# Kernel optimization log

Hardware: AMD Instinct MI355X
Metric: run time of the kernel (lower is better)

The kernel has to match this reference:

```python
import jax, jax.numpy as jnp
import numpy as np

N_NODES = 100000


def _spmm(edge_src, edge_dst, edge_vals, support):
    # out[i] = sum_{e: dst(e)=i} w_e * support[src(e)]  (sparse adj @ support)
    msgs = support[edge_src] * edge_vals[:, None]  # [E, F]
    return jax.ops.segment_sum(msgs, edge_dst, num_segments=N_NODES)


def setup_inputs() -> dict:
    key = jax.random.key(0)
    ks = jax.random.split(key, 8)
    E = 1600000
    feat_dim, nhid, num_class = 256, 64, 16
    x = jax.random.normal(ks[0], (N_NODES, feat_dim), dtype=jnp.float32)
    edge_src = jax.random.randint(ks[1], (E,), 0, N_NODES, dtype=jnp.int32)
    edge_dst = jax.random.randint(ks[2], (E,), 0, N_NODES, dtype=jnp.int32)
    edge_vals = jax.random.uniform(ks[3], (E,), dtype=jnp.float32)
    # Glorot-style init as in the original GraphConvolution.reset_parameters
    W1 = jax.random.normal(ks[4], (feat_dim, nhid), dtype=jnp.float32) / np.sqrt(feat_dim)
    b1 = jnp.zeros((nhid,), dtype=jnp.float32)
    W2 = jax.random.normal(ks[5], (nhid, num_class), dtype=jnp.float32) / np.sqrt(nhid)
    b2 = jnp.zeros((num_class,), dtype=jnp.float32)
    return {"x": x, "edge_src": edge_src, "edge_dst": edge_dst,
            "edge_vals": edge_vals, "W1": W1, "b1": b1, "W2": W2, "b2": b2}


def reference(x, edge_src, edge_dst, edge_vals, W1, b1, W2, b2):
    # gc1: support = x @ W1 ; out = adj @ support + b1 ; relu
    h = jax.nn.relu(_spmm(edge_src, edge_dst, edge_vals, x @ W1) + b1)
    # dropout is identity in eval mode (training=False)
    # gc2
    logits = _spmm(edge_src, edge_dst, edge_vals, h @ W2) + b2
    return jax.nn.log_softmax(logits, axis=1)
```

## Files before the change

kernel.cpp:

```cpp
#include <hip/hip_runtime.h>
#include <hip/hip_fp16.h>

#define N_NODES 100000
#define E_EDGES 1600000
#define F_IN    256
#define F_HID   64
#define F_OUT   16
#define NBKT    391
#define CAP     4608
#define GEMM1_BLOCKS 782
#define PA_BLOCKS    782

typedef _Float16 half8   __attribute__((ext_vector_type(8)));
typedef _Float16 half2v  __attribute__((ext_vector_type(2)));
typedef float    floatx4 __attribute__((ext_vector_type(4)));

__global__ __launch_bounds__(256) void prep_kernel(const float* __restrict__ W1,
                                                   _Float16* __restrict__ W1h,
                                                   int* __restrict__ bucketCursor) {
    const int i = blockIdx.x * 256 + threadIdx.x;
    if (i < NBKT) bucketCursor[i] = 0;
    const int k = i >> 6, n = i & 63;
    const int kb = k >> 5, quad = (k >> 3) & 3, j = k & 7;
    const int nt = n >> 4, ln = n & 15;
    W1h[((kb * 4 + nt) * 64 + quad * 16 + ln) * 8 + j] = (_Float16)W1[i];
}

__global__ __launch_bounds__(256) void gemm1_passA_kernel(const float* __restrict__ x,
                                                          const _Float16* __restrict__ W1h,
                                                          _Float16* __restrict__ support1,
                                                          const int* __restrict__ esrc,
                                                          const int* __restrict__ edst,
                                                          const float* __restrict__ evals,
                                                          int* __restrict__ bucketCursor,
                                                          int2* __restrict__ tmp) {
    __shared__ int hist[NBKT];
    __shared__ int base[NBKT];
    const int t = threadIdx.x;

    if (blockIdx.x >= GEMM1_BLOCKS) {
        const int blk = blockIdx.x - GEMM1_BLOCKS;
        for (int i = t; i < NBKT; i += 256) hist[i] = 0;
        __syncthreads();
        const int base_e = blk * 2048;
        int rks[2][4];
#pragma unroll
        for (int ch = 0; ch < 2; ++ch) {
            const int e0 = base_e + ch * 1024 + t * 4;
            if (e0 < E_EDGES) {
                int4 d4 = *(const int4*)&edst[e0];
                rks[ch][0] = atomicAdd(&hist[d4.x >> 8], 1);
                rks[ch][1] = atomicAdd(&hist[d4.y >> 8], 1);
                rks[ch][2] = atomicAdd(&hist[d4.z >> 8], 1);
                rks[ch][3] = atomicAdd(&hist[d4.w >> 8], 1);
            }
        }
        __syncthreads();
        for (int i = t; i < NBKT; i += 256) {
            const int h = hist[i];
            if (h) base[i] = atomicAdd(&bucketCursor[i], h);
        }
        __syncthreads();
#pragma unroll
        for (int ch = 0; ch < 2; ++ch) {
            const int e0 = base_e + ch * 1024 + t * 4;
            if (e0 < E_EDGES) {
                int4 d4 = *(const int4*)&edst[e0];
                int4 s4 = *(const int4*)&esrc[e0];
                float4 v4 = *(const float4*)&evals[e0];
                const int dd[4] = {d4.x, d4.y, d4.z, d4.w};
                const int ss[4] = {s4.x, s4.y, s4.z, s4.w};
                const float vv[4] = {v4.x, v4.y, v4.z, v4.w};
#pragma unroll
                for (int u = 0; u < 4; ++u) {
                    const int bu = dd[u] >> 8;
                    const int bpos = base[bu] + rks[ch][u];
                    if (bpos < CAP)
                        tmp[(size_t)bu * CAP + bpos] =
                            make_int2(((dd[u] & 255) << 17) | ss[u],
                                      __float_as_int(vv[u]));
                }
            }
        }
        return;
    }

    const int wave = t >> 6;
    const int lane = t & 63;
    const int ln   = lane & 15;
    const int quad = lane >> 4;
    const int row0 = blockIdx.x * 128 + wave * 32;

    const float* xp[2];
#pragma unroll
    for (int mt = 0; mt < 2; ++mt) {
        int r = row0 + mt * 16 + ln;
        if (r > N_NODES - 1) r = N_NODES - 1;
        xp[mt] = x + (size_t)r * F_IN + quad * 8;
    }

    floatx4 acc[2][4] = {};

#pragma unroll 4
    for (int kb = 0; kb < 8; ++kb) {
        half8 a[2];
#pragma unroll
        for (int mt = 0; mt < 2; ++mt) {
            float4 v0 = *(const float4*)(xp[mt] + kb * 32);
            float4 v1 = *(const float4*)(xp[mt] + kb * 32 + 4);
            half8 h;
            h[0] = (_Float16)v0.x; h[1] = (_Float16)v0.y;
            h[2] = (_Float16)v0.z; h[3] = (_Float16)v0.w;
            h[4] = (_Float16)v1.x; h[5] = (_Float16)v1.y;
            h[6] = (_Float16)v1.z; h[7] = (_Float16)v1.w;
            a[mt] = h;
        }
#pragma unroll
        for (int nt = 0; nt < 4; ++nt) {
            half8 b = *(const half8*)&W1h[((size_t)((kb * 4 + nt) * 64 + lane)) * 8];
            acc[0][nt] = __builtin_amdgcn_mfma_f32_16x16x32_f16(a[0], b, acc[0][nt], 0, 0, 0);
            acc[1][nt] = __builtin_amdgcn_mfma_f32_16x16x32_f16(a[1], b, acc[1][nt], 0, 0, 0);
        }
    }

#pragma unroll
    for (int mt = 0; mt < 2; ++mt) {
        const int rbase = row0 + mt * 16 + quad * 4;
#pragma unroll
        for (int r = 0; r < 4; ++r) {
            const int row = rbase + r;
            if (row < N_NODES) {
#pragma unroll
                for (int nt = 0; nt < 4; ++nt)
                    support1[(size_t)row * F_HID + nt * 16 + ln] = (_Float16)acc[mt][nt][r];
            }
        }
    }
}

__global__ __launch_bounds__(256) void passB_kernel(const int2* __restrict__ tmp,
                                                    const int* __restrict__ bucketCursor,
                                                    int2* __restrict__ sorted_edges,
                                                    int* __restrict__ rowstart,
                                                    int* __restrict__ deg) {
    __shared__ int ldeg[256];
    __shared__ int lcur[256];
    __shared__ int s[256];
    const int t = threadIdx.x;
    const int b = blockIdx.x;
    const int beg = b * CAP;
    int cnt = bucketCursor[b];
    if (cnt > CAP) cnt = CAP;

    ldeg[t] = 0;
    __syncthreads();

    for (int p = t; p < cnt; p += 256) {
        int2 r = tmp[beg + p];
        atomicAdd(&ldeg[r.x >> 17], 1);
    }
    __syncthreads();

    const int v = ldeg[t];
    s[t] = v;
    __syncthreads();
#pragma unroll
    for (int off = 1; off < 256; off <<= 1) {
        const int y = (t >= off) ? s[t - off] : 0;
        __syncthreads();
        s[t] += y;
        __syncthreads();
    }
    const int run = s[t] - v;
    lcur[t] = run;
    const int node = b * 256 + t;
    if (node < N_NODES) { rowstart[node] = beg + run; deg[node] = v; }
    __syncthreads();

    for (int p = t; p < cnt; p += 256) {
        int2 r = tmp[beg + p];
        const int pos = beg + atomicAdd(&lcur[r.x >> 17], 1);
        sorted_edges[pos] = make_int2(r.x & 0x1FFFF, r.y);
    }
}

__global__ __launch_bounds__(256) void spmm1_fused_kernel(const int* __restrict__ rowstart,
                                                          const int* __restrict__ deg,
                                                          const int2* __restrict__ sorted_edges,
                                                          const _Float16* __restrict__ support1,
                                                          const float* __restrict__ b1,
                                                          const float* __restrict__ W2,
                                                          _Float16* __restrict__ support2) {
    __shared__ float W2s[64 * 17];
    __shared__ float b1s[64];
    __shared__ __align__(16) float hs[4][64];
    const int t = threadIdx.x;
    for (int i = t; i < 1024; i += 256)
        W2s[(i >> 4) * 17 + (i & 15)] = W2[i];
    if (t < 64) b1s[t] = b1[t];
    __syncthreads();

    const int wave = t >> 6;
    const int lane = t & 63;
    const int node = blockIdx.x * 4 + wave;
    const int c4 = lane & 15;
    const int q  = lane >> 4;

    const int beg = rowstart[node];
    const int cnt = deg[node];

    int   src_l = 0;
    float val_l = 0.f;
    if (lane < cnt) {
        int2 ev = sorted_edges[beg + lane];
        src_l = ev.x;
        val_l = __int_as_float(ev.y);
    }

    half2v a01 = {(_Float16)0, (_Float16)0};
    half2v a23 = {(_Float16)0, (_Float16)0};
    const int kmax  = cnt < 64 ? cnt : 64;
    const int quads = (kmax + 3) >> 2;
    const int qp    = (quads + 3) & ~3;
    for (int k = 0; k < qp; k += 4) {
        float w[4]; uint2 d[4];
#pragma unroll
        for (int u = 0; u < 4; ++u) {
            const int idx = 4 * (k + u) + q;
            const int s2  = __shfl(src_l, idx);
            w[u] = __shfl(val_l, idx);
            d[u] = *(const uint2*)&support1[(s2 << 6) + 4 * c4];
        }
#pragma unroll
        for (int u = 0; u < 4; ++u) {
            const half2v* hp = (const half2v*)&d[u];
            const _Float16 wh = (_Float16)w[u];
            const half2v w2 = {wh, wh};
            a01 += w2 * hp[0];
            a23 += w2 * hp[1];
        }
    }
    for (int k = 64 + q; k < cnt; k += 4) {
        int2 ev = sorted_edges[beg + k];
        const uint2 d = *(const uint2*)&support1[(ev.x << 6) + 4 * c4];
        const half2v* hp = (const half2v*)&d;
        const _Float16 wh = (_Float16)__int_as_float(ev.y);
        const half2v w2 = {wh, wh};
        a01 += w2 * hp[0];
        a23 += w2 * hp[1];
    }

    float acc0 = (float)a01[0], acc1 = (float)a01[1];
    float acc2 = (float)a23[0], acc3 = (float)a23[1];
    acc0 += __shfl_xor(acc0, 16); acc0 += __shfl_xor(acc0, 32);
    acc1 += __shfl_xor(acc1, 16); acc1 += __shfl_xor(acc1, 32);
    acc2 += __shfl_xor(acc2, 16); acc2 += __shfl_xor(acc2, 32);
    acc3 += __shfl_xor(acc3, 16); acc3 += __shfl_xor(acc3, 32);
    if (q == 0) {
        float4 hv;
        hv.x = fmaxf(acc0 + b1s[4 * c4],     0.f);
        hv.y = fmaxf(acc1 + b1s[4 * c4 + 1], 0.f);
        hv.z = fmaxf(acc2 + b1s[4 * c4 + 2], 0.f);
        hv.w = fmaxf(acc3 + b1s[4 * c4 + 3], 0.f);
        *(float4*)&hs[wave][4 * c4] = hv;
    }
    __syncthreads();

    const int ln   = lane & 15;
    const int quad = lane >> 4;
    float o = 0.f;
#pragma unroll
    for (int kk = 0; kk < 16; ++kk) {
        const int k2 = quad * 16 + kk;
        o = fmaf(hs[wave][k2], W2s[k2 * 17 + ln], o);
    }
    o += __shfl_xor(o, 16);
    o += __shfl_xor(o, 32);
    if (quad == 0)
        support2[(size_t)node * F_OUT + ln] = (_Float16)o;
}

__global__ __launch_bounds__(256) void spmm2_fused_kernel(const int* __restrict__ rowstart,
                                                          const int* __restrict__ deg,
                                                          const int2* __restrict__ sorted_edges,
                                                          const _Float16* __restrict__ support2,
                                                          const float* __restrict__ b2,
                                                          float* __restrict__ out) {
    __shared__ float b2s[16];
    const int t = threadIdx.x;
    if (t < 16) b2s[t] = b2[t];
    __syncthreads();

    const int j    = t & 15;
    const int node = blockIdx.x * 16 + (t >> 4);
    const int c = j & 3;
    const int p = j >> 2;

    const int beg = rowstart[node];
    const int cnt = deg[node];

    int   src_a = 0, src_b = 0;
    float val_a = 0.f, val_b = 0.f;
    if (j < cnt)      { int2 ev = sorted_edges[beg + j];      src_a = ev.x; val_a = __int_as_float(ev.y); }
    if (j + 16 < cnt) { int2 ev = sorted_edges[beg + 16 + j]; src_b = ev.x; val_b = __int_as_float(ev.y); }

    half2v a01 = {(_Float16)0, (_Float16)0};
    half2v a23 = {(_Float16)0, (_Float16)0};
    {
        float w[4]; uint2 d[4];
#pragma unroll
        for (int u = 0; u < 4; ++u) {
            const int idx = 4 * u + p;
            const int s2  = __shfl(src_a, idx, 16);
            w[u] = __shfl(val_a, idx, 16);
            d[u] = *(const uint2*)&support2[(s2 << 4) + 4 * c];
        }
#pragma unroll
        for (int u = 0; u < 4; ++u) {
            const half2v* hp = (const half2v*)&d[u];
            const _Float16 wh = (_Float16)w[u];
            const half2v w2 = {wh, wh};
            a01 += w2 * hp[0];
            a23 += w2 * hp[1];
        }
    }
    if (cnt > 16) {
        float w[4]; uint2 d[4];
#pragma unroll
        for (int u = 0; u < 4; ++u) {
            const int idx = 4 * u + p;
            const int s2  = __shfl(src_b, idx, 16);
            w[u] = __shfl(val_b, idx, 16);
            d[u] = *(const uint2*)&support2[(s2 << 4) + 4 * c];
        }
#pragma unroll
        for (int u = 0; u < 4; ++u) {
            const half2v* hp = (const half2v*)&d[u];
            const _Float16 wh = (_Float16)w[u];
            const half2v w2 = {wh, wh};
            a01 += w2 * hp[0];
            a23 += w2 * hp[1];
        }
    }
    for (int k = 32 + p; k < cnt; k += 4) {
        int2 ev = sorted_edges[beg + k];
        const uint2 d = *(const uint2*)&support2[(ev.x << 4) + 4 * c];
        const half2v* hp = (const half2v*)&d;
        const _Float16 wh = (_Float16)__int_as_float(ev.y);
        const half2v w2 = {wh, wh};
        a01 += w2 * hp[0];
        a23 += w2 * hp[1];
    }

    float acc0 = (float)a01[0], acc1 = (float)a01[1];
    float acc2 = (float)a23[0], acc3 = (float)a23[1];
    acc0 += __shfl_xor(acc0, 4, 16); acc0 += __shfl_xor(acc0, 8, 16);
    acc1 += __shfl_xor(acc1, 4, 16); acc1 += __shfl_xor(acc1, 8, 16);
    acc2 += __shfl_xor(acc2, 4, 16); acc2 += __shfl_xor(acc2, 8, 16);
    acc3 += __shfl_xor(acc3, 4, 16); acc3 += __shfl_xor(acc3, 8, 16);

    const float v0 = acc0 + b2s[4 * c];
    const float v1 = acc1 + b2s[4 * c + 1];
    const float v2 = acc2 + b2s[4 * c + 2];
    const float v3 = acc3 + b2s[4 * c + 3];
    float m = fmaxf(fmaxf(v0, v1), fmaxf(v2, v3));
    m = fmaxf(m, __shfl_xor(m, 1, 16));
    m = fmaxf(m, __shfl_xor(m, 2, 16));
    float sum = __expf(v0 - m) + __expf(v1 - m) + __expf(v2 - m) + __expf(v3 - m);
    sum += __shfl_xor(sum, 1, 16);
    sum += __shfl_xor(sum, 2, 16);
    if (p == 0) {
        const float lse = m + __logf(sum);
        float4 o = make_float4(v0 - lse, v1 - lse, v2 - lse, v3 - lse);
        *(float4*)&out[(size_t)node * F_OUT + 4 * c] = o;
    }
}

extern "C" void kernel_launch(void* const* d_in, const int* in_sizes, int n_in,
                              void* d_out, int out_size, void* d_ws, size_t ws_size,
                              hipStream_t stream) {
    const float* x     = (const float*)d_in[0];
    const int*   esrc  = (const int*)  d_in[1];
    const int*   edst  = (const int*)  d_in[2];
    const float* evals = (const float*)d_in[3];
    const float* W1    = (const float*)d_in[4];
    const float* b1    = (const float*)d_in[5];
    const float* W2    = (const float*)d_in[6];
    const float* b2    = (const float*)d_in[7];
    float* out = (float*)d_out;

    char* ws = (char*)d_ws;
    _Float16* support1     = (_Float16*)(ws);
    _Float16* support2     = (_Float16*)(ws + 12800000);
    int2*     tmp          = (int2*)    (ws + 16000000);
    int2*     sorted_edges = (int2*)    (ws + 30413824);
    int*      rowstart     = (int*)     (ws + 44827648);
    int*      deg          = (int*)     (ws + 45227648);
    int*      bucketCursor = (int*)     (ws + 45627648);
    _Float16* W1h          = (_Float16*)(ws + 45629216);

    prep_kernel<<<64, 256, 0, stream>>>(W1, W1h, bucketCursor);
    gemm1_passA_kernel<<<GEMM1_BLOCKS + PA_BLOCKS, 256, 0, stream>>>(
        x, W1h, support1, esrc, edst, evals, bucketCursor, tmp);
    passB_kernel<<<NBKT, 256, 0, stream>>>(tmp, bucketCursor, sorted_edges, rowstart, deg);
    spmm1_fused_kernel<<<N_NODES / 4, 256, 0, stream>>>(rowstart, deg, sorted_edges,
                                                        support1, b1, W2, support2);
    spmm2_fused_kernel<<<N_NODES / 16, 256, 0, stream>>>(rowstart, deg, sorted_edges,
                                                         support2, b2, out);
}
```

Baseline: 285.5 us.

## Merge five launches into one persistent cooperative kernel with grid syncs

Replaces the prep, gemm/partition, bucket-sort, and two SpMM kernels with one cooperative persistent kernel. Blocks loop over the former grids and separate the phases with grid.sync(). The rowstart and deg arrays are packed into a single int2 array. The aim is to remove per-launch overhead and inter-kernel gaps, at the cost of grid-wide barrier latency, a possibly occupancy-limited grid size, and load imbalance within phases.

```diff
diff --git a/kernel.cpp b/kernel.cpp
--- a/kernel.cpp
+++ b/kernel.cpp
@@ -1,5 +1,8 @@
 #include <hip/hip_runtime.h>
 #include <hip/hip_fp16.h>
+#include <hip/hip_cooperative_groups.h>
+
+namespace cg = cooperative_groups;
 
 #define N_NODES 100000
 #define E_EDGES 1600000
@@ -15,364 +18,368 @@
 typedef _Float16 half2v  __attribute__((ext_vector_type(2)));
 typedef float    floatx4 __attribute__((ext_vector_type(4)));
 
-__global__ __launch_bounds__(256) void prep_kernel(const float* __restrict__ W1,
-                                                   _Float16* __restrict__ W1h,
-                                                   int* __restrict__ bucketCursor) {
-    const int i = blockIdx.x * 256 + threadIdx.x;
-    if (i < NBKT) bucketCursor[i] = 0;
-    const int k = i >> 6, n = i & 63;
-    const int kb = k >> 5, quad = (k >> 3) & 3, j = k & 7;
-    const int nt = n >> 4, ln = n & 15;
-    W1h[((kb * 4 + nt) * 64 + quad * 16 + ln) * 8 + j] = (_Float16)W1[i];
-}
-
-__global__ __launch_bounds__(256) void gemm1_passA_kernel(const float* __restrict__ x,
-                                                          const _Float16* __restrict__ W1h,
-                                                          _Float16* __restrict__ support1,
-                                                          const int* __restrict__ esrc,
-                                                          const int* __restrict__ edst,
-                                                          const float* __restrict__ evals,
-                                                          int* __restrict__ bucketCursor,
-                                                          int2* __restrict__ tmp) {
-    __shared__ int hist[NBKT];
-    __shared__ int base[NBKT];
+__global__ __launch_bounds__(256, 8) void mega_kernel(
+        const float* __restrict__ x,
+        const int* __restrict__ esrc,
+        const int* __restrict__ edst,
+        const float* __restrict__ evals,
+        const float* __restrict__ W1,
+        const float* __restrict__ b1,
+        const float* __restrict__ W2,
+        const float* __restrict__ b2,
+        float* __restrict__ out,
+        _Float16* __restrict__ support1,
+        _Float16* __restrict__ support2,
+        int2* __restrict__ tmp,
+        int2* __restrict__ sorted_edges,
+        int2* __restrict__ rowdeg,
+        int* __restrict__ bucketCursor,
+        _Float16* __restrict__ W1h) {
+    __shared__ __align__(16) char lds[5632];
     const int t = threadIdx.x;
-
-    if (blockIdx.x >= GEMM1_BLOCKS) {
-        const int blk = blockIdx.x - GEMM1_BLOCKS;
-        for (int i = t; i < NBKT; i += 256) hist[i] = 0;
+    const int nblk = gridDim.x;
+    cg::grid_group grid = cg::this_grid();
+
+    for (int i = blockIdx.x * 256 + t; i < 16384; i += nblk * 256) {
+        if (i < NBKT) bucketCursor[i] = 0;
+        const int k = i >> 6, n = i & 63;
+        const int kb = k >> 5, quad = (k >> 3) & 3, j = k & 7;
+        const int nt = n >> 4, ln = n & 15;
+        W1h[((kb * 4 + nt) * 64 + quad * 16 + ln) * 8 + j] = (_Float16)W1[i];
+    }
+    grid.sync();
+
+    for (int vb = blockIdx.x; vb < GEMM1_BLOCKS + PA_BLOCKS; vb += nblk) {
+        if (vb >= GEMM1_BLOCKS) {
+            int* hist = (int*)lds;
+            int* base = hist + NBKT;
+            const int blk = vb - GEMM1_BLOCKS;
+            for (int i = t; i < NBKT; i += 256) hist[i] = 0;
+            __syncthreads();
+            const int base_e = blk * 2048;
+            int rks[2][4];
+#pragma unroll
+            for (int ch = 0; ch < 2; ++ch) {
+                const int e0 = base_e + ch * 1024 + t * 4;
+                if (e0 < E_EDGES) {
+                    int4 d4 = *(const int4*)&edst[e0];
+                    rks[ch][0] = atomicAdd(&hist[d4.x >> 8], 1);
+                    rks[ch][1] = atomicAdd(&hist[d4.y >> 8], 1);
+                    rks[ch][2] = atomicAdd(&hist[d4.z >> 8], 1);
+                    rks[ch][3] = atomicAdd(&hist[d4.w >> 8], 1);
+                }
+            }
+            __syncthreads();
+            for (int i = t; i < NBKT; i += 256) {
+                const int h = hist[i];
+                if (h) base[i] = atomicAdd(&bucketCursor[i], h);
+            }
+            __syncthreads();
+#pragma unroll
+            for (int ch = 0; ch < 2; ++ch) {
+                const int e0 = base_e + ch * 1024 + t * 4;
+                if (e0 < E_EDGES) {
+                    int4 d4 = *(const int4*)&edst[e0];
+                    int4 s4 = *(const int4*)&esrc[e0];
+                    float4 v4 = *(const float4*)&evals[e0];
+                    const int dd[4] = {d4.x, d4.y, d4.z, d4.w};
+                    const int ss[4] = {s4.x, s4.y, s4.z, s4.w};
+                    const float vv[4] = {v4.x, v4.y, v4.z, v4.w};
+#pragma unroll
+                    for (int u = 0; u < 4; ++u) {
+                        const int bu = dd[u] >> 8;
+                        const int bpos = base[bu] + rks[ch][u];
+                        if (bpos < CAP)
+                            tmp[(size_t)bu * CAP + bpos] =
+                                make_int2(((dd[u] & 255) << 17) | ss[u],
+                                          __float_as_int(vv[u]));
+                    }
+                }
+            }
+            __syncthreads();
+        } else {
+            const int wave = t >> 6;
+            const int lane = t & 63;
+            const int ln   = lane & 15;
+            const int quad = lane >> 4;
+            const int row0 = vb * 128 + wave * 32;
+
+            const float* xp[2];
+#pragma unroll
+            for (int mt = 0; mt < 2; ++mt) {
+                int r = row0 + mt * 16 + ln;
+                if (r > N_NODES - 1) r = N_NODES - 1;
+                xp[mt] = x + (size_t)r * F_IN + quad * 8;
+            }
+
+            floatx4 acc[2][4] = {};
+
+#pragma unroll 4
+            for (int kb = 0; kb < 8; ++kb) {
+                half8 a[2];
+#pragma unroll
+                for (int mt = 0; mt < 2; ++mt) {
+                    float4 v0 = *(const float4*)(xp[mt] + kb * 32);
+                    float4 v1 = *(const float4*)(xp[mt] + kb * 32 + 4);
+                    half8 h;
+                    h[0] = (_Float16)v0.x; h[1] = (_Float16)v0.y;
+                    h[2] = (_Float16)v0.z; h[3] = (_Float16)v0.w;
+                    h[4] = (_Float16)v1.x; h[5] = (_Float16)v1.y;
+                    h[6] = (_Float16)v1.z; h[7] = (_Float16)v1.w;
+                    a[mt] = h;
+                }
+#pragma unroll
+                for (int nt = 0; nt < 4; ++nt) {
+                    half8 bb = *(const half8*)&W1h[((size_t)((kb * 4 + nt) * 64 + lane)) * 8];
+                    acc[0][nt] = __builtin_amdgcn_mfma_f32_16x16x32_f16(a[0], bb, acc[0][nt], 0, 0, 0);
+                    acc[1][nt] = __builtin_amdgcn_mfma_f32_16x16x32_f16(a[1], bb, acc[1][nt], 0, 0, 0);
+                }
+            }
+
+#pragma unroll
+            for (int mt = 0; mt < 2; ++mt) {
+                const int rbase = row0 + mt * 16 + quad * 4;
+#pragma unroll
+                for (int r = 0; r < 4; ++r) {
+                    const int row = rbase + r;
+                    if (row < N_NODES) {
+#pragma unroll
+                        for (int nt = 0; nt < 4; ++nt)
+                            support1[(size_t)row * F_HID + nt * 16 + ln] = (_Float16)acc[mt][nt][r];
+                    }
+                }
+            }
+        }
+    }
+    grid.sync();
+
+    {
+        int* ldeg = (int*)lds;
+        int* lcur = ldeg + 256;
+        int* s    = lcur + 256;
+        for (int b = blockIdx.x; b < NBKT; b += nblk) {
+            const int beg = b * CAP;
+            int cnt = bucketCursor[b];
+            if (cnt > CAP) cnt = CAP;
+
+            ldeg[t] = 0;
+            __syncthreads();
+
+            for (int p = t; p < cnt; p += 256) {
+                int2 r = tmp[beg + p];
+                atomicAdd(&ldeg[r.x >> 17], 1);
+            }
+            __syncthreads();
+
+            const int v = ldeg[t];
+            s[t] = v;
+            __syncthreads();
+#pragma unroll
+            for (int off = 1; off < 256; off <<= 1) {
+                const int y = (t >= off) ? s[t - off] : 0;
+                __syncthreads();
+                s[t] += y;
+                __syncthreads();
+            }
+            const int run = s[t] - v;
+            lcur[t] = run;
+            const int node = b * 256 + t;
+            if (node < N_NODES) rowdeg[node] = make_int2(beg + run, v);
+            __syncthreads();
+
+            for (int p = t; p < cnt; p += 256) {
+                int2 r = tmp[beg + p];
+                const int pos = beg + atomicAdd(&lcur[r.x >> 17], 1);
+                sorted_edges[pos] = make_int2(r.x & 0x1FFFF, r.y);
+            }
+            __syncthreads();
+        }
+    }
+    grid.sync();
+
+    {
+        float* W2s = (float*)lds;
+        float* b1s = (float*)(lds + 4352);
+        float* hs  = (float*)(lds + 4608);
+        for (int i = t; i < 1024; i += 256)
+            W2s[(i >> 4) * 17 + (i & 15)] = W2[i];
+        if (t < 64) b1s[t] = b1[t];
         __syncthreads();
-        const int base_e = blk * 2048;
-        int rks[2][4];
-#pragma unroll
-        for (int ch = 0; ch < 2; ++ch) {
-            const int e0 = base_e + ch * 1024 + t * 4;
-            if (e0 < E_EDGES) {
-                int4 d4 = *(const int4*)&edst[e0];
-                rks[ch][0] = atomicAdd(&hist[d4.x >> 8], 1);
-                rks[ch][1] = atomicAdd(&hist[d4.y >> 8], 1);
-                rks[ch][2] = atomicAdd(&hist[d4.z >> 8], 1);
-                rks[ch][3] = atomicAdd(&hist[d4.w >> 8], 1);
-            }
+
+        const int wave = t >> 6;
+        const int lane = t & 63;
+        const int c4 = lane & 15;
+        const int q  = lane >> 4;
+        const int ln   = lane & 15;
+        const int quad = lane >> 4;
+
+        for (int g = blockIdx.x; g < 25000; g += nblk) {
+            const int node = g * 4 + wave;
+            const int2 rd = rowdeg[node];
+            const int beg = rd.x;
+            const int cnt = rd.y;
+
+            int   src_l = 0;
+            float val_l = 0.f;
+            if (lane < cnt) {
+                int2 ev = sorted_edges[beg + lane];
+                src_l = ev.x;
+                val_l = __int_as_float(ev.y);
+            }
+
+            half2v a01 = {(_Float16)0, (_Float16)0};
+            half2v a23 = {(_Float16)0, (_Float16)0};
+            const int kmax  = cnt < 64 ? cnt : 64;
+            const int quads = (kmax + 3) >> 2;
+            const int qp    = (quads + 3) & ~3;
+            for (int k = 0; k < qp; k += 4) {
+                float w[4]; uint2 d[4];
+#pragma unroll
+                for (int u = 0; u < 4; ++u) {
+                    const int idx = 4 * (k + u) + q;
+                    const int s2  = __shfl(src_l, idx);
+                    w[u] = __shfl(val_l, idx);
+                    d[u] = *(const uint2*)&support1[(s2 << 6) + 4 * c4];
+                }
+#pragma unroll
+                for (int u = 0; u < 4; ++u) {
+                    const half2v* hp = (const half2v*)&d[u];
+                    const _Float16 wh = (_Float16)w[u];
+                    const half2v w2 = {wh, wh};
+                    a01 += w2 * hp[0];
+                    a23 += w2 * hp[1];
+                }
+            }
+            for (int k = 64 + q; k < cnt; k += 4) {
+                int2 ev = sorted_edges[beg + k];
+                const uint2 d = *(const uint2*)&support1[(ev.x << 6) + 4 * c4];
+                const half2v* hp = (const half2v*)&d;
+                const _Float16 wh = (_Float16)__int_as_float(ev.y);
+                const half2v w2 = {wh, wh};
+                a01 += w2 * hp[0];
+                a23 += w2 * hp[1];
+            }
+
+            float acc0 = (float)a01[0], acc1 = (float)a01[1];
+            float acc2 = (float)a23[0], acc3 = (float)a23[1];
+            acc0 += __shfl_xor(acc0, 16); acc0 += __shfl_xor(acc0, 32);
+            acc1 += __shfl_xor(acc1, 16); acc1 += __shfl_xor(acc1, 32);
+            acc2 += __shfl_xor(acc2, 16); acc2 += __shfl_xor(acc2, 32);
+            acc3 += __shfl_xor(acc3, 16); acc3 += __shfl_xor(acc3, 32);
+            if (q == 0) {
+                float4 hv;
+                hv.x = fmaxf(acc0 + b1s[4 * c4],     0.f);
+                hv.y = fmaxf(acc1 + b1s[4 * c4 + 1], 0.f);
+                hv.z = fmaxf(acc2 + b1s[4 * c4 + 2], 0.f);
+                hv.w = fmaxf(acc3 + b1s[4 * c4 + 3], 0.f);
+                *(float4*)&hs[wave * 64 + 4 * c4] = hv;
+            }
+
+            float o = 0.f;
+#pragma unroll
+            for (int kk = 0; kk < 16; ++kk) {
+                const int k2 = quad * 16 + kk;
+                o = fmaf(hs[wave * 64 + k2], W2s[k2 * 17 + ln], o);
+            }
+            o += __shfl_xor(o, 16);
+            o += __shfl_xor(o, 32);
+            if (quad == 0)
+                support2[(size_t)node * F_OUT + ln] = (_Float16)o;
         }
+    }
+    grid.sync();
+
+    {
+        float* b2s = (float*)lds;
+        if (t < 16) b2s[t] = b2[t];
         __syncthreads();
-        for (int i = t; i < NBKT; i += 256) {
-            const int h = hist[i];
-            if (h) base[i] = atomicAdd(&bucketCursor[i], h);
+
+        const int j = t & 15;
+        const int c = j & 3;
+        const int p = j >> 2;
+
+        for (int g = blockIdx.x; g < 6250; g += nblk) {
+            const int node = g * 16 + (t >> 4);
+            const int2 rd = rowdeg[node];
+            const int beg = rd.x;
+            const int cnt = rd.y;
+
+            int   src_a = 0, src_b = 0;
+            float val_a = 0.f, val_b = 0.f;
+            if (j < cnt)      { int2 ev = sorted_edges[beg + j];      src_a = ev.x; val_a = __int_as_float(ev.y); }
+            if (j + 16 < cnt) { int2 ev = sorted_edges[beg + 16 + j]; src_b = ev.x; val_b = __int_as_float(ev.y); }
+
+            half2v a01 = {(_Float16)0, (_Float16)0};
+            half2v a23 = {(_Float16)0, (_Float16)0};
+            {
+                float w[4]; uint2 d[4];
+#pragma unroll
+                for (int u = 0; u < 4; ++u) {
+                    const int idx = 4 * u + p;
+                    const int s2  = __shfl(src_a, idx, 16);
+                    w[u] = __shfl(val_a, idx, 16);
+                    d[u] = *(const uint2*)&support2[(s2 << 4) + 4 * c];
+                }
+#pragma unroll
+                for (int u = 0; u < 4; ++u) {
+                    const half2v* hp = (const half2v*)&d[u];
+                    const _Float16 wh = (_Float16)w[u];
+                    const half2v w2 = {wh, wh};
+                    a01 += w2 * hp[0];
+                    a23 += w2 * hp[1];
+                }
+            }
+            if (cnt > 16) {
+                float w[4]; uint2 d[4];
+#pragma unroll
+                for (int u = 0; u < 4; ++u) {
+                    const int idx = 4 * u + p;
+                    const int s2  = __shfl(src_b, idx, 16);
+                    w[u] = __shfl(val_b, idx, 16);
+                    d[u] = *(const uint2*)&support2[(s2 << 4) + 4 * c];
+                }
+#pragma unroll
+                for (int u = 0; u < 4; ++u) {
+                    const half2v* hp = (const half2v*)&d[u];
+                    const _Float16 wh = (_Float16)w[u];
+                    const half2v w2 = {wh, wh};
+                    a01 += w2 * hp[0];
+                    a23 += w2 * hp[1];
+                }
+            }
+            for (int k = 32 + p; k < cnt; k += 4) {
+                int2 ev = sorted_edges[beg + k];
+                const uint2 d = *(const uint2*)&support2[(ev.x << 4) + 4 * c];
+                const half2v* hp = (const half2v*)&d;
+                const _Float16 wh = (_Float16)__int_as_float(ev.y);
+                const half2v w2 = {wh, wh};
+                a01 += w2 * hp[0];
+                a23 += w2 * hp[1];
+            }
+
+            float acc0 = (float)a01[0], acc1 = (float)a01[1];
+            float acc2 = (float)a23[0], acc3 = (float)a23[1];
+            acc0 += __shfl_xor(acc0, 4, 16); acc0 += __shfl_xor(acc0, 8, 16);
+            acc1 += __shfl_xor(acc1, 4, 16); acc1 += __shfl_xor(acc1, 8, 16);
+            acc2 += __shfl_xor(acc2, 4, 16); acc2 += __shfl_xor(acc2, 8, 16);
+            acc3 += __shfl_xor(acc3, 4, 16); acc3 += __shfl_xor(acc3, 8, 16);
+
+            const float v0 = acc0 + b2s[4 * c];
+            const float v1 = acc1 + b2s[4 * c + 1];
+            const float v2 = acc2 + b2s[4 * c + 2];
+            const float v3 = acc3 + b2s[4 * c + 3];
+            float m = fmaxf(fmaxf(v0, v1), fmaxf(v2, v3));
+            m = fmaxf(m, __shfl_xor(m, 1, 16));
+            m = fmaxf(m, __shfl_xor(m, 2, 16));
+            float sum = __expf(v0 - m) + __expf(v1 - m) + __expf(v2 - m) + __expf(v3 - m);
+            sum += __shfl_xor(sum, 1, 16);
+            sum += __shfl_xor(sum, 2, 16);
+            if (p == 0) {
+                const float lse = m + __logf(sum);
+                float4 o = make_float4(v0 - lse, v1 - lse, v2 - lse, v3 - lse);
+                *(float4*)&out[(size_t)node * F_OUT + 4 * c] = o;
+            }
         }
-        __syncthreads();
-#pragma unroll
-        for (int ch = 0; ch < 2; ++ch) {
-            const int e0 = base_e + ch * 1024 + t * 4;
-            if (e0 < E_EDGES) {
-                int4 d4 = *(const int4*)&edst[e0];
-                int4 s4 = *(const int4*)&esrc[e0];
-                float4 v4 = *(const float4*)&evals[e0];
-                const int dd[4] = {d4.x, d4.y, d4.z, d4.w};
-                const int ss[4] = {s4.x, s4.y, s4.z, s4.w};
-                const float vv[4] = {v4.x, v4.y, v4.z, v4.w};
-#pragma unroll
-                for (int u = 0; u < 4; ++u) {
-                    const int bu = dd[u] >> 8;
-                    const int bpos = base[bu] + rks[ch][u];
-                    if (bpos < CAP)
-                        tmp[(size_t)bu * CAP + bpos] =
-                            make_int2(((dd[u] & 255) << 17) | ss[u],
-                                      __float_as_int(vv[u]));
-                }
-            }
-        }
-        return;
-    }
-
-    const int wave = t >> 6;
-    const int lane = t & 63;
-    const int ln   = lane & 15;
-    const int quad = lane >> 4;
-    const int row0 = blockIdx.x * 128 + wave * 32;
-
-    const float* xp[2];
-#pragma unroll
-    for (int mt = 0; mt < 2; ++mt) {
-        int r = row0 + mt * 16 + ln;
-        if (r > N_NODES - 1) r = N_NODES - 1;
-        xp[mt] = x + (size_t)r * F_IN + quad * 8;
-    }
-
-    floatx4 acc[2][4] = {};
-
-#pragma unroll 4
-    for (int kb = 0; kb < 8; ++kb) {
-        half8 a[2];
-#pragma unroll
-        for (int mt = 0; mt < 2; ++mt) {
-            float4 v0 = *(const float4*)(xp[mt] + kb * 32);
-            float4 v1 = *(const float4*)(xp[mt] + kb * 32 + 4);
-            half8 h;
-            h[0] = (_Float16)v0.x; h[1] = (_Float16)v0.y;
-            h[2] = (_Float16)v0.z; h[3] = (_Float16)v0.w;
-            h[4] = (_Float16)v1.x; h[5] = (_Float16)v1.y;
-            h[6] = (_Float16)v1.z; h[7] = (_Float16)v1.w;
-            a[mt] = h;
-        }
-#pragma unroll
-        for (int nt = 0; nt < 4; ++nt) {
-            half8 b = *(const half8*)&W1h[((size_t)((kb * 4 + nt) * 64 + lane)) * 8];
-            acc[0][nt] = __builtin_amdgcn_mfma_f32_16x16x32_f16(a[0], b, acc[0][nt], 0, 0, 0);
-            acc[1][nt] = __builtin_amdgcn_mfma_f32_16x16x32_f16(a[1], b, acc[1][nt], 0, 0, 0);
-        }
-    }
-
-#pragma unroll
-    for (int mt = 0; mt < 2; ++mt) {
-        const int rbase = row0 + mt * 16 + quad * 4;
-#pragma unroll
-        for (int r = 0; r < 4; ++r) {
-            const int row = rbase + r;
-            if (row < N_NODES) {
-#pragma unroll
-                for (int nt = 0; nt < 4; ++nt)
-                    support1[(size_t)row * F_HID + nt * 16 + ln] = (_Float16)acc[mt][nt][r];
-            }
-        }
-    }
-}
-
-__global__ __launch_bounds__(256) void passB_kernel(const int2* __restrict__ tmp,
-                                                    const int* __restrict__ bucketCursor,
-                                                    int2* __restrict__ sorted_edges,
-                                                    int* __restrict__ rowstart,
-                                                    int* __restrict__ deg) {
-    __shared__ int ldeg[256];
-    __shared__ int lcur[256];
-    __shared__ int s[256];
-    const int t = threadIdx.x;
-    const int b = blockIdx.x;
-    const int beg = b * CAP;
-    int cnt = bucketCursor[b];
-    if (cnt > CAP) cnt = CAP;
-
-    ldeg[t] = 0;
-    __syncthreads();
-
-    for (int p = t; p < cnt; p += 256) {
-        int2 r = tmp[beg + p];
-        atomicAdd(&ldeg[r.x >> 17], 1);
-    }
-    __syncthreads();
-
-    const int v = ldeg[t];
-    s[t] = v;
-    __syncthreads();
-#pragma unroll
-    for (int off = 1; off < 256; off <<= 1) {
-        const int y = (t >= off) ? s[t - off] : 0;
-        __syncthreads();
-        s[t] += y;
-        __syncthreads();
-    }
-    const int run = s[t] - v;
-    lcur[t] = run;
-    const int node = b * 256 + t;
-    if (node < N_NODES) { rowstart[node] = beg + run; deg[node] = v; }
-    __syncthreads();
-
-    for (int p = t; p < cnt; p += 256) {
-        int2 r = tmp[beg + p];
-        const int pos = beg + atomicAdd(&lcur[r.x >> 17], 1);
-        sorted_edges[pos] = make_int2(r.x & 0x1FFFF, r.y);
-    }
-}
-
-__global__ __launch_bounds__(256) void spmm1_fused_kernel(const int* __restrict__ rowstart,
-                                                          const int* __restrict__ deg,
-                                                          const int2* __restrict__ sorted_edges,
-                                                          const _Float16* __restrict__ support1,
-                                                          const float* __restrict__ b1,
-                                                          const float* __restrict__ W2,
-                                                          _Float16* __restrict__ support2) {
-    __shared__ float W2s[64 * 17];
-    __shared__ float b1s[64];
-    __shared__ __align__(16) float hs[4][64];
-    const int t = threadIdx.x;
-    for (int i = t; i < 1024; i += 256)
-        W2s[(i >> 4) * 17 + (i & 15)] = W2[i];
-    if (t < 64) b1s[t] = b1[t];
-    __syncthreads();
-
-    const int wave = t >> 6;
-    const int lane = t & 63;
-    const int node = blockIdx.x * 4 + wave;
-    const int c4 = lane & 15;
-    const int q  = lane >> 4;
-
-    const int beg = rowstart[node];
-    const int cnt = deg[node];
-
-    int   src_l = 0;
-    float val_l = 0.f;
-    if (lane < cnt) {
-        int2 ev = sorted_edges[beg + lane];
-        src_l = ev.x;
-        val_l = __int_as_float(ev.y);
-    }
-
-    half2v a01 = {(_Float16)0, (_Float16)0};
-    half2v a23 = {(_Float16)0, (_Float16)0};
-    const int kmax  = cnt < 64 ? cnt : 64;
-    const int quads = (kmax + 3) >> 2;
-    const int qp    = (quads + 3) & ~3;
-    for (int k = 0; k < qp; k += 4) {
-        float w[4]; uint2 d[4];
-#pragma unroll
-        for (int u = 0; u < 4; ++u) {
-            const int idx = 4 * (k + u) + q;
-            const int s2  = __shfl(src_l, idx);
-            w[u] = __shfl(val_l, idx);
-            d[u] = *(const uint2*)&support1[(s2 << 6) + 4 * c4];
-        }
-#pragma unroll
-        for (int u = 0; u < 4; ++u) {
-            const half2v* hp = (const half2v*)&d[u];
-            const _Float16 wh = (_Float16)w[u];
-            const half2v w2 = {wh, wh};
-            a01 += w2 * hp[0];
-            a23 += w2 * hp[1];
-        }
-    }
-    for (int k = 64 + q; k < cnt; k += 4) {
-        int2 ev = sorted_edges[beg + k];
-        const uint2 d = *(const uint2*)&support1[(ev.x << 6) + 4 * c4];
-        const half2v* hp = (const half2v*)&d;
-        const _Float16 wh = (_Float16)__int_as_float(ev.y);
-        const half2v w2 = {wh, wh};
-        a01 += w2 * hp[0];
-        a23 += w2 * hp[1];
-    }
-
-    float acc0 = (float)a01[0], acc1 = (float)a01[1];
-    float acc2 = (float)a23[0], acc3 = (float)a23[1];
-    acc0 += __shfl_xor(acc0, 16); acc0 += __shfl_xor(acc0, 32);
-    acc1 += __shfl_xor(acc1, 16); acc1 += __shfl_xor(acc1, 32);
-    acc2 += __shfl_xor(acc2, 16); acc2 += __shfl_xor(acc2, 32);
-    acc3 += __shfl_xor(acc3, 16); acc3 += __shfl_xor(acc3, 32);
-    if (q == 0) {
-        float4 hv;
-        hv.x = fmaxf(acc0 + b1s[4 * c4],     0.f);
-        hv.y = fmaxf(acc1 + b1s[4 * c4 + 1], 0.f);
-        hv.z = fmaxf(acc2 + b1s[4 * c4 + 2], 0.f);
-        hv.w = fmaxf(acc3 + b1s[4 * c4 + 3], 0.f);
-        *(float4*)&hs[wave][4 * c4] = hv;
-    }
-    __syncthreads();
-
-    const int ln   = lane & 15;
-    const int quad = lane >> 4;
-    float o = 0.f;
-#pragma unroll
-    for (int kk = 0; kk < 16; ++kk) {
-        const int k2 = quad * 16 + kk;
-        o = fmaf(hs[wave][k2], W2s[k2 * 17 + ln], o);
-    }
-    o += __shfl_xor(o, 16);
-    o += __shfl_xor(o, 32);
-    if (quad == 0)
-        support2[(size_t)node * F_OUT + ln] = (_Float16)o;
-}
-
-__global__ __launch_bounds__(256) void spmm2_fused_kernel(const int* __restrict__ rowstart,
-                                                          const int* __restrict__ deg,
-                                                          const int2* __restrict__ sorted_edges,
-                                                          const _Float16* __restrict__ support2,
-                                                          const float* __restrict__ b2,
-                                                          float* __restrict__ out) {
-    __shared__ float b2s[16];
-    const int t = threadIdx.x;
-    if (t < 16) b2s[t] = b2[t];
-    __syncthreads();
-
-    const int j    = t & 15;
-    const int node = blockIdx.x * 16 + (t >> 4);
-    const int c = j & 3;
-    const int p = j >> 2;
-
-    const int beg = rowstart[node];
-    const int cnt = deg[node];
-
-    int   src_a = 0, src_b = 0;
-    float val_a = 0.f, val_b = 0.f;
-    if (j < cnt)      { int2 ev = sorted_edges[beg + j];      src_a = ev.x; val_a = __int_as_float(ev.y); }
-    if (j + 16 < cnt) { int2 ev = sorted_edges[beg + 16 + j]; src_b = ev.x; val_b = __int_as_float(ev.y); }
-
-    half2v a01 = {(_Float16)0, (_Float16)0};
-    half2v a23 = {(_Float16)0, (_Float16)0};
-    {
-        float w[4]; uint2 d[4];
-#pragma unroll
-        for (int u = 0; u < 4; ++u) {
-            const int idx = 4 * u + p;
-            const int s2  = __shfl(src_a, idx, 16);
-            w[u] = __shfl(val_a, idx, 16);
-            d[u] = *(const uint2*)&support2[(s2 << 4) + 4 * c];
-        }
-#pragma unroll
-        for (int u = 0; u < 4; ++u) {
-            const half2v* hp = (const half2v*)&d[u];
-            const _Float16 wh = (_Float16)w[u];
-            const half2v w2 = {wh, wh};
-            a01 += w2 * hp[0];
-            a23 += w2 * hp[1];
-        }
-    }
-    if (cnt > 16) {
-        float w[4]; uint2 d[4];
-#pragma unroll
-        for (int u = 0; u < 4; ++u) {
-            const int idx = 4 * u + p;
-            const int s2  = __shfl(src_b, idx, 16);
-            w[u] = __shfl(val_b, idx, 16);
-            d[u] = *(const uint2*)&support2[(s2 << 4) + 4 * c];
-        }
-#pragma unroll
-        for (int u = 0; u < 4; ++u) {
-            const half2v* hp = (const half2v*)&d[u];
-            const _Float16 wh = (_Float16)w[u];
-            const half2v w2 = {wh, wh};
-            a01 += w2 * hp[0];
-            a23 += w2 * hp[1];
-        }
-    }
-    for (int k = 32 + p; k < cnt; k += 4) {
-        int2 ev = sorted_edges[beg + k];
-        const uint2 d = *(const uint2*)&support2[(ev.x << 4) + 4 * c];
-        const half2v* hp = (const half2v*)&d;
-        const _Float16 wh = (_Float16)__int_as_float(ev.y);
-        const half2v w2 = {wh, wh};
-        a01 += w2 * hp[0];
-        a23 += w2 * hp[1];
-    }
-
-    float acc0 = (float)a01[0], acc1 = (float)a01[1];
-    float acc2 = (float)a23[0], acc3 = (float)a23[1];
-    acc0 += __shfl_xor(acc0, 4, 16); acc0 += __shfl_xor(acc0, 8, 16);
-    acc1 += __shfl_xor(acc1, 4, 16); acc1 += __shfl_xor(acc1, 8, 16);
-    acc2 += __shfl_xor(acc2, 4, 16); acc2 += __shfl_xor(acc2, 8, 16);
-    acc3 += __shfl_xor(acc3, 4, 16); acc3 += __shfl_xor(acc3, 8, 16);
-
-    const float v0 = acc0 + b2s[4 * c];
-    const float v1 = acc1 + b2s[4 * c + 1];
-    const float v2 = acc2 + b2s[4 * c + 2];
-    const float v3 = acc3 + b2s[4 * c + 3];
-    float m = fmaxf(fmaxf(v0, v1), fmaxf(v2, v3));
-    m = fmaxf(m, __shfl_xor(m, 1, 16));
-    m = fmaxf(m, __shfl_xor(m, 2, 16));
-    float sum = __expf(v0 - m) + __expf(v1 - m) + __expf(v2 - m) + __expf(v3 - m);
-    sum += __shfl_xor(sum, 1, 16);
-    sum += __shfl_xor(sum, 2, 16);
-    if (p == 0) {
-        const float lse = m + __logf(sum);
-        float4 o = make_float4(v0 - lse, v1 - lse, v2 - lse, v3 - lse);
-        *(float4*)&out[(size_t)node * F_OUT + 4 * c] = o;
     }
 }
 
@@ -394,17 +401,29 @@
     _Float16* support2     = (_Float16*)(ws + 12800000);
     int2*     tmp          = (int2*)    (ws + 16000000);
     int2*     sorted_edges = (int2*)    (ws + 30413824);
-    int*      rowstart     = (int*)     (ws + 44827648);
-    int*      deg          = (int*)     (ws + 45227648);
+    int2*     rowdeg       = (int2*)    (ws + 44827648);
     int*      bucketCursor = (int*)     (ws + 45627648);
     _Float16* W1h          = (_Float16*)(ws + 45629216);
 
-    prep_kernel<<<64, 256, 0, stream>>>(W1, W1h, bucketCursor);
-    gemm1_passA_kernel<<<GEMM1_BLOCKS + PA_BLOCKS, 256, 0, stream>>>(
-        x, W1h, support1, esrc, edst, evals, bucketCursor, tmp);
-    passB_kernel<<<NBKT, 256, 0, stream>>>(tmp, bucketCursor, sorted_edges, rowstart, deg);
-    spmm1_fused_kernel<<<N_NODES / 4, 256, 0, stream>>>(rowstart, deg, sorted_edges,
-                                                        support1, b1, W2, support2);
-    spmm2_fused_kernel<<<N_NODES / 16, 256, 0, stream>>>(rowstart, deg, sorted_edges,
-                                                         support2, b2, out);
+    static int grid = 0;
+    if (grid == 0) {
+        int perCU = 0;
+        hipOccupancyMaxActiveBlocksPerMultiprocessor(&perCU, mega_kernel, 256, 0);
+        if (perCU < 1) perCU = 1;
+        int dev = 0;
+        hipGetDevice(&dev);
+        hipDeviceProp_t prop;
+        hipGetDeviceProperties(&prop, dev);
+        grid = perCU * prop.multiProcessorCount;
+        if (grid > 2048) grid = 2048;
+        if (grid < 64) grid = 64;
+    }
+
+    void* args[] = {(void*)&x, (void*)&esrc, (void*)&edst, (void*)&evals,
+                    (void*)&W1, (void*)&b1, (void*)&W2, (void*)&b2,
+                    (void*)&out, (void*)&support1, (void*)&support2,
+                    (void*)&tmp, (void*)&sorted_edges, (void*)&rowdeg,
+                    (void*)&bucketCursor, (void*)&W1h};
+    hipLaunchCooperativeKernel((const void*)mega_kernel, dim3(grid), dim3(256),
+                               args, 0, stream);
 }
```

Result: slower. 756.6 us (+165.0%).
